# Kernel tuning notes

Hardware: AMD Instinct MI355X
Metric: run time of the kernel (lower is better)

## Reference

```python
import jax, jax.numpy as jnp
import numpy as np

NUM_HEADS = 16

def setup_inputs() -> dict:
    key = jax.random.key(0)
    ks = jax.random.split(key, 7)
    B, N, D = 2, 2048, 1024
    x = jax.random.normal(ks[0], (B, N, D), dtype=jnp.float32)
    gamma = jax.random.uniform(ks[1], (B, NUM_HEADS), dtype=jnp.float32)
    dist_matrix = jax.random.uniform(ks[2], (N, N), dtype=jnp.float32)
    W_qkv = jax.random.normal(ks[3], (D, 3 * D), dtype=jnp.float32) * (D ** -0.5)
    b_qkv = jnp.zeros((3 * D,), dtype=jnp.float32)
    W_proj = jax.random.normal(ks[4], (D, D), dtype=jnp.float32) * (D ** -0.5)
    b_proj = jnp.zeros((D,), dtype=jnp.float32)
    return {"x": x, "gamma": gamma, "dist_matrix": dist_matrix,
            "W_qkv": W_qkv, "b_qkv": b_qkv, "W_proj": W_proj, "b_proj": b_proj}

def reference(x, gamma, dist_matrix, W_qkv, b_qkv, W_proj, b_proj):
    B, N, D = x.shape
    H = NUM_HEADS
    hd = D // H
    scale = D ** -0.5  # standard_scale=False -> dim**-0.5
    # qkv projection: [B,N,3D] -> [3,B,H,N,hd]
    qkv = (x @ W_qkv + b_qkv).reshape(B, N, 3, H, hd).transpose(2, 0, 3, 1, 4)
    q, k, v = qkv[0], qkv[1], qkv[2]
    # scores with zoom bias: [B,H,N,N]
    scores = jnp.einsum('bhnd,bhmd->bhnm', q, k) * scale
    scores = scores - gamma[:, :, None, None] * dist_matrix[None, None, :, :]
    attn = jax.nn.softmax(scores, axis=-1)
    out = jnp.einsum('bhnm,bhmd->bhnd', attn, v)  # [B,H,N,hd]
    out = out.transpose(0, 2, 1, 3).reshape(B, N, D)
    return out @ W_proj + b_proj
```

## Files before the change

kernel.cpp:

```cpp
#include <hip/hip_runtime.h>
#include <cstdint>
#include <cstddef>

#define HD 64
#define NH 16
#define BATCH 2
#define SEQ 2048
#define DIM 1024
#define SCALE 0.03125f
#define LOG2E 1.4426950408889634f
#define QSCALE (SCALE * LOG2E)
#define NT (SEQ / 64)

typedef short bf16x8 __attribute__((ext_vector_type(8)));
typedef float f32x4 __attribute__((ext_vector_type(4)));
typedef unsigned u32x2 __attribute__((ext_vector_type(2)));
typedef unsigned u32x4 __attribute__((ext_vector_type(4)));

#define GL16(gp, lp) __builtin_amdgcn_global_load_lds( \
    (const __attribute__((address_space(1))) unsigned int*)(gp), \
    (__attribute__((address_space(3))) unsigned int*)(lp), 16, 0, 0)

static __device__ __forceinline__ unsigned short f2bf(float f) {
  union { float f; unsigned u; } a; a.f = f;
  unsigned r = a.u + 0x7fffu + ((a.u >> 16) & 1u);
  return (unsigned short)(r >> 16);
}

static __device__ __forceinline__ f32x4 zero4() {
  f32x4 z; z[0] = 0.f; z[1] = 0.f; z[2] = 0.f; z[3] = 0.f; return z;
}

__global__ void convert_x(const float* __restrict__ in, unsigned short* __restrict__ out, int n4) {
  int i = blockIdx.x * blockDim.x + threadIdx.x;
  if (i < n4) {
    float4 v = reinterpret_cast<const float4*>(in)[i];
    ushort4 o;
    o.x = f2bf(v.x); o.y = f2bf(v.y); o.z = f2bf(v.z); o.w = f2bf(v.w);
    reinterpret_cast<ushort4*>(out)[i] = o;
  }
}

__global__ void transpose_convert(const float* __restrict__ in, unsigned short* __restrict__ out,
                                  int R, int C) {
  __shared__ float tile[32][33];
  int bx = blockIdx.x * 32;
  int by = blockIdx.y * 32;
  int tx = threadIdx.x, ty = threadIdx.y;
  #pragma unroll
  for (int i = 0; i < 32; i += 8)
    tile[ty + i][tx] = in[(size_t)(by + ty + i) * C + bx + tx];
  __syncthreads();
  #pragma unroll
  for (int i = 0; i < 32; i += 8)
    out[(size_t)(bx + ty + i) * R + by + tx] = f2bf(tile[tx][ty + i]);
}

__global__ __launch_bounds__(256) void gemm128(
    const unsigned short* __restrict__ A, const unsigned short* __restrict__ Bt,
    const float* __restrict__ bias, int K, int mode,
    unsigned short* __restrict__ qo, unsigned short* __restrict__ ko,
    unsigned short* __restrict__ vo, float* __restrict__ outf) {
  __shared__ __attribute__((aligned(16))) unsigned short As[128 * 64];
  __shared__ __attribute__((aligned(16))) unsigned short Bs[128 * 64];
  const int tid = threadIdx.x;
  const int lane = tid & 63, w = tid >> 6;
  const int lo = lane & 15, hi = lane >> 4;
  const int wm = w >> 1, wn = w & 1;
  const int m0 = blockIdx.y * 128, n0 = blockIdx.x * 128;
  const int srow = tid >> 3, scol = (tid & 7) * 8;
  const unsigned short* abase = A + (size_t)(m0 + srow) * K + scol;
  const unsigned short* bbase = Bt + (size_t)(n0 + srow) * K + scol;

  f32x4 acc[4][4];
  #pragma unroll
  for (int mr = 0; mr < 4; ++mr)
    #pragma unroll
    for (int nr = 0; nr < 4; ++nr) acc[mr][nr] = zero4();

  const int nkt = K / 64;
  for (int kt = 0; kt < nkt; ++kt) {
    const unsigned short* ak = abase + kt * 64;
    const unsigned short* bk = bbase + kt * 64;
    #pragma unroll
    for (int i = 0; i < 4; ++i) {
      GL16(ak + (size_t)(32 * i) * K, &As[(w * 64 + 256 * i) * 8]);
      GL16(bk + (size_t)(32 * i) * K, &Bs[(w * 64 + 256 * i) * 8]);
    }
    __syncthreads();
    __builtin_amdgcn_s_setprio(1);
    #pragma unroll
    for (int kc = 0; kc < 2; ++kc) {
      bf16x8 af[4], bfr[4];
      #pragma unroll
      for (int mr = 0; mr < 4; ++mr)
        af[mr] = *reinterpret_cast<const bf16x8*>(
            &As[(wm * 64 + mr * 16 + lo) * 64 + kc * 32 + hi * 8]);
      #pragma unroll
      for (int nr = 0; nr < 4; ++nr)
        bfr[nr] = *reinterpret_cast<const bf16x8*>(
            &Bs[(wn * 64 + nr * 16 + lo) * 64 + kc * 32 + hi * 8]);
      #pragma unroll
      for (int mr = 0; mr < 4; ++mr)
        #pragma unroll
        for (int nr = 0; nr < 4; ++nr)
          acc[mr][nr] = __builtin_amdgcn_mfma_f32_16x16x32_bf16(af[mr], bfr[nr], acc[mr][nr], 0, 0, 0);
    }
    __builtin_amdgcn_s_setprio(0);
    __syncthreads();
  }

  #pragma unroll
  for (int nr = 0; nr < 4; ++nr) {
    const int gcol = n0 + wn * 64 + nr * 16 + lo;
    const float bv = bias[gcol];
    #pragma unroll
    for (int mr = 0; mr < 4; ++mr)
      #pragma unroll
      for (int j = 0; j < 4; ++j) {
        const int grow = m0 + wm * 64 + mr * 16 + hi * 4 + j;
        float val = acc[mr][nr][j] + bv;
        if (mode == 0) {
          int which = gcol >> 10;
          int hh = (gcol >> 6) & 15;
          int d = gcol & 63;
          int bb = grow >> 11;
          int n = grow & 2047;
          if (which == 0) {
            qo[((size_t)(bb * NH + hh) * SEQ + n) * HD + d] = f2bf(val * QSCALE);
          } else if (which == 1) {
            ko[((size_t)(bb * NH + hh) * SEQ + n) * HD + d] = f2bf(val);
          } else {
            vo[((size_t)(bb * NH + hh) * HD + d) * SEQ + n] = f2bf(val);
          }
        } else {
          outf[(size_t)grow * DIM + gcol] = val;
        }
      }
  }
}

__global__ __launch_bounds__(256, 4) void attn_kernel(
    const unsigned short* __restrict__ qb, const unsigned short* __restrict__ kb,
    const unsigned short* __restrict__ vtb, const float* __restrict__ gamma,
    const float* __restrict__ dist, unsigned short* __restrict__ ab) {
  __shared__ __attribute__((aligned(16))) unsigned short Ks[2][64 * 64];
  __shared__ __attribute__((aligned(16))) unsigned short Vt[2][64 * 64];
  __shared__ __attribute__((aligned(16))) unsigned short Ps[4 * 16 * 64];
  const int tid = threadIdx.x;
  const int lane = tid & 63;
  const int w = tid >> 6;
  const int lo = lane & 15;
  const int hi = lane >> 4;
  const int idx = blockIdx.x;
  const int bh = idx & 31;
  const int qt = idx >> 5;
  const int b = bh >> 4, h = bh & 15;
  const int qrow0 = qt * 64 + w * 16;
  const float g2 = gamma[bh] * LOG2E;

  const size_t base = (size_t)bh * SEQ * HD;
  const size_t vtbase = (size_t)bh * HD * SEQ;

  bf16x8 qf[2];
  #pragma unroll
  for (int kc = 0; kc < 2; ++kc)
    qf[kc] = *reinterpret_cast<const bf16x8*>(
        &qb[base + (size_t)(qrow0 + lo) * HD + kc * 32 + hi * 8]);

  const float* drow = dist + (size_t)(qrow0 + lo) * SEQ + hi * 4;

  f32x4 o[4];
  #pragma unroll
  for (int db = 0; db < 4; ++db) o[db] = zero4();
  float m_run = -INFINITY;
  float l_run = 0.f;

  const int srow = tid >> 3;
  const int schunk = (tid & 7) ^ (srow & 7);
  const unsigned short* ksrc0 = kb + base + (size_t)srow * HD + schunk * 8;
  const unsigned short* ksrc1 = ksrc0 + (size_t)32 * HD;
  const unsigned short* vsrc0 = vtb + vtbase + (size_t)srow * SEQ + schunk * 8;
  const unsigned short* vsrc1 = vsrc0 + (size_t)32 * SEQ;

  unsigned short* const psw = &Ps[w * 1024 + lo * 64];

  f32x4 dvA[4], dvB[4];

  GL16(ksrc0, &Ks[0][w * 512]);
  GL16(ksrc1, &Ks[0][2048 + w * 512]);
  GL16(vsrc0, &Vt[0][w * 512]);
  GL16(vsrc1, &Vt[0][2048 + w * 512]);
  #pragma unroll
  for (int nb = 0; nb < 4; ++nb)
    dvA[nb] = *reinterpret_cast<const f32x4*>(drow + nb * 16);
  __syncthreads();

#define TILE_BODY(CUR, NXT, MT, DVC, DVN)                                              \
  {                                                                                    \
    if ((MT) + 1 < NT) {                                                               \
      const int m1_ = ((MT) + 1) * 64;                                                 \
      GL16(ksrc0 + (size_t)m1_ * HD, &Ks[NXT][w * 512]);                               \
      GL16(ksrc1 + (size_t)m1_ * HD, &Ks[NXT][2048 + w * 512]);                        \
      GL16(vsrc0 + m1_, &Vt[NXT][w * 512]);                                            \
      GL16(vsrc1 + m1_, &Vt[NXT][2048 + w * 512]);                                     \
      _Pragma("unroll")                                                                \
      for (int nb = 0; nb < 4; ++nb)                                                   \
        DVN[nb] = *reinterpret_cast<const f32x4*>(drow + m1_ + nb * 16);               \
    }                                                                                  \
    f32x4 s[4];                                                                        \
    _Pragma("unroll")                                                                  \
    for (int nb = 0; nb < 4; ++nb) s[nb] = zero4();                                    \
    __builtin_amdgcn_s_setprio(1);                                                     \
    _Pragma("unroll")                                                                  \
    for (int nb = 0; nb < 4; ++nb)                                                     \
      _Pragma("unroll")                                                                \
      for (int kc = 0; kc < 2; ++kc) {                                                 \
        bf16x8 kf = *reinterpret_cast<const bf16x8*>(                                  \
            &Ks[CUR][(nb * 16 + lo) * 64 + ((kc * 4 + hi) ^ (lo & 7)) * 8]);           \
        s[nb] = __builtin_amdgcn_mfma_f32_16x16x32_bf16(kf, qf[kc], s[nb], 0, 0, 0);   \
      }                                                                                \
    __builtin_amdgcn_s_setprio(0);                                                     \
    float pm = -INFINITY;                                                              \
    _Pragma("unroll")                                                                  \
    for (int nb = 0; nb < 4; ++nb)                                                     \
      _Pragma("unroll")                                                                \
      for (int j = 0; j < 4; ++j) {                                                    \
        float v_ = __builtin_fmaf(-g2, DVC[nb][j], s[nb][j]);                          \
        s[nb][j] = v_;                                                                 \
        pm = fmaxf(pm, v_);                                                            \
      }                                                                                \
    pm = fmaxf(pm, __shfl_xor(pm, 16, 64));                                            \
    pm = fmaxf(pm, __shfl_xor(pm, 32, 64));                                            \
    if (!__all(pm <= m_run + 8.0f)) {                                                  \
      float mn_ = fmaxf(m_run, pm);                                                    \
      float corr_ = exp2f(m_run - mn_);                                                \
      m_run = mn_;                                                                     \
      l_run *= corr_;                                                                  \
      _Pragma("unroll")                                                                \
      for (int db = 0; db < 4; ++db) {                                                 \
        o[db][0] *= corr_; o[db][1] *= corr_;                                          \
        o[db][2] *= corr_; o[db][3] *= corr_;                                          \
      }                                                                                \
    }                                                                                  \
    float psum = 0.f;                                                                  \
    _Pragma("unroll")                                                                  \
    for (int nb = 0; nb < 4; ++nb) {                                                   \
      float p0 = exp2f(s[nb][0] - m_run);                                              \
      float p1 = exp2f(s[nb][1] - m_run);                                              \
      float p2 = exp2f(s[nb][2] - m_run);                                              \
      float p3 = exp2f(s[nb][3] - m_run);                                              \
      psum += (p0 + p1) + (p2 + p3);                                                   \
      unsigned pk0, pk1;                                                               \
      asm("v_cvt_pk_bf16_f32 %0, %1, %2" : "=v"(pk0) : "v"(p0), "v"(p1));              \
      asm("v_cvt_pk_bf16_f32 %0, %1, %2" : "=v"(pk1) : "v"(p2), "v"(p3));              \
      u32x2 pw_; pw_[0] = pk0; pw_[1] = pk1;                                           \
      *reinterpret_cast<u32x2*>(&psw[(((nb << 2) + hi) ^ lo) * 4]) = pw_;              \
    }                                                                                  \
    psum += __shfl_xor(psum, 16, 64);                                                  \
    psum += __shfl_xor(psum, 32, 64);                                                  \
    l_run += psum;                                                                     \
    __builtin_amdgcn_s_setprio(1);                                                     \
    _Pragma("unroll")                                                                  \
    for (int kc = 0; kc < 2; ++kc) {                                                   \
      u32x2 ra = *reinterpret_cast<const u32x2*>(&psw[(((kc << 3) + hi * 2) ^ lo) * 4]); \
      u32x2 rb = *reinterpret_cast<const u32x2*>(&psw[(((kc << 3) + hi * 2 + 1) ^ lo) * 4]); \
      u32x4 t_; t_[0] = ra[0]; t_[1] = ra[1]; t_[2] = rb[0]; t_[3] = rb[1];            \
      bf16x8 pf = __builtin_bit_cast(bf16x8, t_);                                      \
      _Pragma("unroll")                                                                \
      for (int db = 0; db < 4; ++db) {                                                 \
        bf16x8 vtf = *reinterpret_cast<const bf16x8*>(                                 \
            &Vt[CUR][(db * 16 + lo) * 64 + ((kc * 4 + hi) ^ (lo & 7)) * 8]);           \
        o[db] = __builtin_amdgcn_mfma_f32_16x16x32_bf16(vtf, pf, o[db], 0, 0, 0);      \
      }                                                                                \
    }                                                                                  \
    __builtin_amdgcn_s_setprio(0);                                                     \
    __syncthreads();                                                                   \
  }

  for (int mt = 0; mt < NT; mt += 2) {
    TILE_BODY(0, 1, mt, dvA, dvB)
    TILE_BODY(1, 0, mt + 1, dvB, dvA)
  }
#undef TILE_BODY

  {
    float rl = 1.0f / l_run;
    size_t row = (size_t)b * SEQ + qrow0 + lo;
    #pragma unroll
    for (int db = 0; db < 4; ++db) {
      ushort4 w4;
      w4.x = f2bf(o[db][0] * rl);
      w4.y = f2bf(o[db][1] * rl);
      w4.z = f2bf(o[db][2] * rl);
      w4.w = f2bf(o[db][3] * rl);
      *reinterpret_cast<ushort4*>(&ab[row * DIM + h * HD + db * 16 + hi * 4]) = w4;
    }
  }
}

extern "C" void kernel_launch(void* const* d_in, const int* in_sizes, int n_in,
                              void* d_out, int out_size, void* d_ws, size_t ws_size,
                              hipStream_t stream) {
  const float* x     = (const float*)d_in[0];
  const float* gamma = (const float*)d_in[1];
  const float* dist  = (const float*)d_in[2];
  const float* Wqkv  = (const float*)d_in[3];
  const float* bqkv  = (const float*)d_in[4];
  const float* Wproj = (const float*)d_in[5];
  const float* bproj = (const float*)d_in[6];
  float* out = (float*)d_out;

  char* ws = (char*)d_ws;
  unsigned short* xb     = (unsigned short*)(ws);
  unsigned short* wqkvt  = (unsigned short*)(ws + 8388608);
  unsigned short* wprojt = (unsigned short*)(ws + 14680064);
  unsigned short* qbuf   = (unsigned short*)(ws + 16777216);
  unsigned short* kbuf   = (unsigned short*)(ws + 25165824);
  unsigned short* vtbuf  = (unsigned short*)(ws + 33554432);
  unsigned short* abuf   = (unsigned short*)(ws + 41943040);

  convert_x<<<4096, 256, 0, stream>>>(x, xb, (BATCH * SEQ * DIM) / 4);
  transpose_convert<<<dim3(96, 32), dim3(32, 8), 0, stream>>>(Wqkv, wqkvt, DIM, 3 * DIM);
  transpose_convert<<<dim3(32, 32), dim3(32, 8), 0, stream>>>(Wproj, wprojt, DIM, DIM);
  gemm128<<<dim3(24, 32), 256, 0, stream>>>(xb, wqkvt, bqkv, DIM, 0, qbuf, kbuf, vtbuf, nullptr);
  attn_kernel<<<(SEQ / 64) * BATCH * NH, 256, 0, stream>>>(qbuf, kbuf, vtbuf, gamma, dist, abuf);
  gemm128<<<dim3(8, 32), 256, 0, stream>>>(abuf, wprojt, bproj, DIM, 1, nullptr, nullptr, nullptr, out);
}
```

Baseline: 172.4 us.

## Switch attention to 32x32x16 MFMA with register-resident P via permlane swap

```diff
diff --git a/kernel.cpp b/kernel.cpp
--- a/kernel.cpp
+++ b/kernel.cpp
@@ -14,7 +14,7 @@
 
 typedef short bf16x8 __attribute__((ext_vector_type(8)));
 typedef float f32x4 __attribute__((ext_vector_type(4)));
-typedef unsigned u32x2 __attribute__((ext_vector_type(2)));
+typedef float f32x16 __attribute__((ext_vector_type(16)));
 typedef unsigned u32x4 __attribute__((ext_vector_type(4)));
 
 #define GL16(gp, lp) __builtin_amdgcn_global_load_lds( \
@@ -140,39 +140,38 @@
   }
 }
 
-__global__ __launch_bounds__(256, 4) void attn_kernel(
+__global__ __launch_bounds__(256, 2) void attn_kernel(
     const unsigned short* __restrict__ qb, const unsigned short* __restrict__ kb,
     const unsigned short* __restrict__ vtb, const float* __restrict__ gamma,
     const float* __restrict__ dist, unsigned short* __restrict__ ab) {
   __shared__ __attribute__((aligned(16))) unsigned short Ks[2][64 * 64];
   __shared__ __attribute__((aligned(16))) unsigned short Vt[2][64 * 64];
-  __shared__ __attribute__((aligned(16))) unsigned short Ps[4 * 16 * 64];
   const int tid = threadIdx.x;
   const int lane = tid & 63;
   const int w = tid >> 6;
-  const int lo = lane & 15;
-  const int hi = lane >> 4;
+  const int q5 = lane & 31;
+  const int h5 = lane >> 5;
   const int idx = blockIdx.x;
   const int bh = idx & 31;
   const int qt = idx >> 5;
   const int b = bh >> 4, h = bh & 15;
-  const int qrow0 = qt * 64 + w * 16;
+  const int qrow0 = qt * 128 + w * 32;
   const float g2 = gamma[bh] * LOG2E;
 
   const size_t base = (size_t)bh * SEQ * HD;
   const size_t vtbase = (size_t)bh * HD * SEQ;
 
-  bf16x8 qf[2];
-  #pragma unroll
-  for (int kc = 0; kc < 2; ++kc)
-    qf[kc] = *reinterpret_cast<const bf16x8*>(
-        &qb[base + (size_t)(qrow0 + lo) * HD + kc * 32 + hi * 8]);
-
-  const float* drow = dist + (size_t)(qrow0 + lo) * SEQ + hi * 4;
-
-  f32x4 o[4];
-  #pragma unroll
-  for (int db = 0; db < 4; ++db) o[db] = zero4();
+  bf16x8 qf[4];
+  #pragma unroll
+  for (int ks = 0; ks < 4; ++ks)
+    qf[ks] = *reinterpret_cast<const bf16x8*>(
+        &qb[base + (size_t)(qrow0 + q5) * HD + ks * 16 + h5 * 8]);
+
+  const float* drow = dist + (size_t)(qrow0 + q5) * SEQ + 4 * h5;
+
+  f32x16 o[2];
+  #pragma unroll
+  for (int i = 0; i < 16; ++i) { o[0][i] = 0.f; o[1][i] = 0.f; }
   float m_run = -INFINITY;
   float l_run = 0.f;
 
@@ -183,119 +182,140 @@
   const unsigned short* vsrc0 = vtb + vtbase + (size_t)srow * SEQ + schunk * 8;
   const unsigned short* vsrc1 = vsrc0 + (size_t)32 * SEQ;
 
-  unsigned short* const psw = &Ps[w * 1024 + lo * 64];
-
-  f32x4 dvA[4], dvB[4];
+  f32x4 dv[2][4];
+  #pragma unroll
+  for (int blk = 0; blk < 2; ++blk)
+    #pragma unroll
+    for (int rp = 0; rp < 4; ++rp)
+      dv[blk][rp] = *reinterpret_cast<const f32x4*>(drow + 32 * blk + 8 * rp);
 
   GL16(ksrc0, &Ks[0][w * 512]);
   GL16(ksrc1, &Ks[0][2048 + w * 512]);
   GL16(vsrc0, &Vt[0][w * 512]);
   GL16(vsrc1, &Vt[0][2048 + w * 512]);
-  #pragma unroll
-  for (int nb = 0; nb < 4; ++nb)
-    dvA[nb] = *reinterpret_cast<const f32x4*>(drow + nb * 16);
   __syncthreads();
 
-#define TILE_BODY(CUR, NXT, MT, DVC, DVN)                                              \
-  {                                                                                    \
-    if ((MT) + 1 < NT) {                                                               \
-      const int m1_ = ((MT) + 1) * 64;                                                 \
-      GL16(ksrc0 + (size_t)m1_ * HD, &Ks[NXT][w * 512]);                               \
-      GL16(ksrc1 + (size_t)m1_ * HD, &Ks[NXT][2048 + w * 512]);                        \
-      GL16(vsrc0 + m1_, &Vt[NXT][w * 512]);                                            \
-      GL16(vsrc1 + m1_, &Vt[NXT][2048 + w * 512]);                                     \
-      _Pragma("unroll")                                                                \
-      for (int nb = 0; nb < 4; ++nb)                                                   \
-        DVN[nb] = *reinterpret_cast<const f32x4*>(drow + m1_ + nb * 16);               \
-    }                                                                                  \
-    f32x4 s[4];                                                                        \
-    _Pragma("unroll")                                                                  \
-    for (int nb = 0; nb < 4; ++nb) s[nb] = zero4();                                    \
-    __builtin_amdgcn_s_setprio(1);                                                     \
-    _Pragma("unroll")                                                                  \
-    for (int nb = 0; nb < 4; ++nb)                                                     \
-      _Pragma("unroll")                                                                \
-      for (int kc = 0; kc < 2; ++kc) {                                                 \
-        bf16x8 kf = *reinterpret_cast<const bf16x8*>(                                  \
-            &Ks[CUR][(nb * 16 + lo) * 64 + ((kc * 4 + hi) ^ (lo & 7)) * 8]);           \
-        s[nb] = __builtin_amdgcn_mfma_f32_16x16x32_bf16(kf, qf[kc], s[nb], 0, 0, 0);   \
-      }                                                                                \
-    __builtin_amdgcn_s_setprio(0);                                                     \
-    float pm = -INFINITY;                                                              \
-    _Pragma("unroll")                                                                  \
-    for (int nb = 0; nb < 4; ++nb)                                                     \
-      _Pragma("unroll")                                                                \
-      for (int j = 0; j < 4; ++j) {                                                    \
-        float v_ = __builtin_fmaf(-g2, DVC[nb][j], s[nb][j]);                          \
-        s[nb][j] = v_;                                                                 \
-        pm = fmaxf(pm, v_);                                                            \
-      }                                                                                \
-    pm = fmaxf(pm, __shfl_xor(pm, 16, 64));                                            \
-    pm = fmaxf(pm, __shfl_xor(pm, 32, 64));                                            \
-    if (!__all(pm <= m_run + 8.0f)) {                                                  \
-      float mn_ = fmaxf(m_run, pm);                                                    \
-      float corr_ = exp2f(m_run - mn_);                                                \
-      m_run = mn_;                                                                     \
-      l_run *= corr_;                                                                  \
-      _Pragma("unroll")                                                                \
-      for (int db = 0; db < 4; ++db) {                                                 \
-        o[db][0] *= corr_; o[db][1] *= corr_;                                          \
-        o[db][2] *= corr_; o[db][3] *= corr_;                                          \
-      }                                                                                \
-    }                                                                                  \
-    float psum = 0.f;                                                                  \
-    _Pragma("unroll")                                                                  \
-    for (int nb = 0; nb < 4; ++nb) {                                                   \
-      float p0 = exp2f(s[nb][0] - m_run);                                              \
-      float p1 = exp2f(s[nb][1] - m_run);                                              \
-      float p2 = exp2f(s[nb][2] - m_run);                                              \
-      float p3 = exp2f(s[nb][3] - m_run);                                              \
-      psum += (p0 + p1) + (p2 + p3);                                                   \
-      unsigned pk0, pk1;                                                               \
-      asm("v_cvt_pk_bf16_f32 %0, %1, %2" : "=v"(pk0) : "v"(p0), "v"(p1));              \
-      asm("v_cvt_pk_bf16_f32 %0, %1, %2" : "=v"(pk1) : "v"(p2), "v"(p3));              \
-      u32x2 pw_; pw_[0] = pk0; pw_[1] = pk1;                                           \
-      *reinterpret_cast<u32x2*>(&psw[(((nb << 2) + hi) ^ lo) * 4]) = pw_;              \
-    }                                                                                  \
-    psum += __shfl_xor(psum, 16, 64);                                                  \
-    psum += __shfl_xor(psum, 32, 64);                                                  \
-    l_run += psum;                                                                     \
-    __builtin_amdgcn_s_setprio(1);                                                     \
-    _Pragma("unroll")                                                                  \
-    for (int kc = 0; kc < 2; ++kc) {                                                   \
-      u32x2 ra = *reinterpret_cast<const u32x2*>(&psw[(((kc << 3) + hi * 2) ^ lo) * 4]); \
-      u32x2 rb = *reinterpret_cast<const u32x2*>(&psw[(((kc << 3) + hi * 2 + 1) ^ lo) * 4]); \
-      u32x4 t_; t_[0] = ra[0]; t_[1] = ra[1]; t_[2] = rb[0]; t_[3] = rb[1];            \
-      bf16x8 pf = __builtin_bit_cast(bf16x8, t_);                                      \
-      _Pragma("unroll")                                                                \
-      for (int db = 0; db < 4; ++db) {                                                 \
-        bf16x8 vtf = *reinterpret_cast<const bf16x8*>(                                 \
-            &Vt[CUR][(db * 16 + lo) * 64 + ((kc * 4 + hi) ^ (lo & 7)) * 8]);           \
-        o[db] = __builtin_amdgcn_mfma_f32_16x16x32_bf16(vtf, pf, o[db], 0, 0, 0);      \
-      }                                                                                \
-    }                                                                                  \
-    __builtin_amdgcn_s_setprio(0);                                                     \
-    __syncthreads();                                                                   \
-  }
-
-  for (int mt = 0; mt < NT; mt += 2) {
-    TILE_BODY(0, 1, mt, dvA, dvB)
-    TILE_BODY(1, 0, mt + 1, dvB, dvA)
-  }
-#undef TILE_BODY
+  for (int mt = 0; mt < NT; ++mt) {
+    const int cur = mt & 1;
+    if (mt + 1 < NT) {
+      const int m1 = (mt + 1) * 64;
+      GL16(ksrc0 + (size_t)m1 * HD, &Ks[cur ^ 1][w * 512]);
+      GL16(ksrc1 + (size_t)m1 * HD, &Ks[cur ^ 1][2048 + w * 512]);
+      GL16(vsrc0 + m1, &Vt[cur ^ 1][w * 512]);
+      GL16(vsrc1 + m1, &Vt[cur ^ 1][2048 + w * 512]);
+    }
+
+    f32x16 s[2];
+    #pragma unroll
+    for (int i = 0; i < 16; ++i) { s[0][i] = 0.f; s[1][i] = 0.f; }
+    __builtin_amdgcn_s_setprio(1);
+    #pragma unroll
+    for (int blk = 0; blk < 2; ++blk)
+      #pragma unroll
+      for (int ks = 0; ks < 4; ++ks) {
+        bf16x8 kf = *reinterpret_cast<const bf16x8*>(
+            &Ks[cur][(blk * 32 + q5) * 64 + ((ks * 2 + h5) ^ (q5 & 7)) * 8]);
+        s[blk] = __builtin_amdgcn_mfma_f32_32x32x16_bf16(kf, qf[ks], s[blk], 0, 0, 0);
+      }
+    __builtin_amdgcn_s_setprio(0);
+
+    float mx[8];
+    #pragma unroll
+    for (int blk = 0; blk < 2; ++blk)
+      #pragma unroll
+      for (int rp = 0; rp < 4; ++rp) {
+        float v0 = __builtin_fmaf(-g2, dv[blk][rp][0], s[blk][rp * 4 + 0]);
+        float v1 = __builtin_fmaf(-g2, dv[blk][rp][1], s[blk][rp * 4 + 1]);
+        float v2 = __builtin_fmaf(-g2, dv[blk][rp][2], s[blk][rp * 4 + 2]);
+        float v3 = __builtin_fmaf(-g2, dv[blk][rp][3], s[blk][rp * 4 + 3]);
+        s[blk][rp * 4 + 0] = v0; s[blk][rp * 4 + 1] = v1;
+        s[blk][rp * 4 + 2] = v2; s[blk][rp * 4 + 3] = v3;
+        mx[blk * 4 + rp] = fmaxf(fmaxf(v0, v1), fmaxf(v2, v3));
+      }
+    float pm = fmaxf(fmaxf(fmaxf(mx[0], mx[1]), fmaxf(mx[2], mx[3])),
+                     fmaxf(fmaxf(mx[4], mx[5]), fmaxf(mx[6], mx[7])));
+    pm = fmaxf(pm, __shfl_xor(pm, 32, 64));
+
+    if (mt + 1 < NT) {
+      const float* dn = drow + (mt + 1) * 64;
+      #pragma unroll
+      for (int blk = 0; blk < 2; ++blk)
+        #pragma unroll
+        for (int rp = 0; rp < 4; ++rp)
+          dv[blk][rp] = *reinterpret_cast<const f32x4*>(dn + 32 * blk + 8 * rp);
+    }
+
+    if (!__all(pm <= m_run + 8.0f)) {
+      float mn = fmaxf(m_run, pm);
+      float corr = exp2f(m_run - mn);
+      m_run = mn;
+      l_run *= corr;
+      #pragma unroll
+      for (int i = 0; i < 16; ++i) { o[0][i] *= corr; o[1][i] *= corr; }
+    }
+
+    float psum = 0.f;
+    unsigned u[2][4][2];
+    #pragma unroll
+    for (int blk = 0; blk < 2; ++blk)
+      #pragma unroll
+      for (int rp = 0; rp < 4; ++rp) {
+        float p0 = exp2f(s[blk][rp * 4 + 0] - m_run);
+        float p1 = exp2f(s[blk][rp * 4 + 1] - m_run);
+        float p2 = exp2f(s[blk][rp * 4 + 2] - m_run);
+        float p3 = exp2f(s[blk][rp * 4 + 3] - m_run);
+        psum += (p0 + p1) + (p2 + p3);
+        asm("v_cvt_pk_bf16_f32 %0, %1, %2" : "=v"(u[blk][rp][0]) : "v"(p0), "v"(p1));
+        asm("v_cvt_pk_bf16_f32 %0, %1, %2" : "=v"(u[blk][rp][1]) : "v"(p2), "v"(p3));
+      }
+    psum += __shfl_xor(psum, 32, 64);
+    l_run += psum;
+
+    unsigned pu[4][4];
+    #pragma unroll
+    for (int blk = 0; blk < 2; ++blk)
+      #pragma unroll
+      for (int jp = 0; jp < 2; ++jp) {
+        unsigned a0 = u[blk][0][jp], b0 = u[blk][1][jp];
+        asm("v_permlane32_swap_b32 %0, %1" : "+v"(a0), "+v"(b0));
+        pu[2 * blk][jp] = a0; pu[2 * blk][2 + jp] = b0;
+        unsigned a1 = u[blk][2][jp], b1 = u[blk][3][jp];
+        asm("v_permlane32_swap_b32 %0, %1" : "+v"(a1), "+v"(b1));
+        pu[2 * blk + 1][jp] = a1; pu[2 * blk + 1][2 + jp] = b1;
+      }
+
+    __builtin_amdgcn_s_setprio(1);
+    #pragma unroll
+    for (int ks = 0; ks < 4; ++ks) {
+      u32x4 t; t[0] = pu[ks][0]; t[1] = pu[ks][1]; t[2] = pu[ks][2]; t[3] = pu[ks][3];
+      bf16x8 pf = __builtin_bit_cast(bf16x8, t);
+      #pragma unroll
+      for (int db = 0; db < 2; ++db) {
+        bf16x8 vtf = *reinterpret_cast<const bf16x8*>(
+            &Vt[cur][(db * 32 + q5) * 64 + ((ks * 2 + h5) ^ (q5 & 7)) * 8]);
+        o[db] = __builtin_amdgcn_mfma_f32_32x32x16_bf16(vtf, pf, o[db], 0, 0, 0);
+      }
+    }
+    __builtin_amdgcn_s_setprio(0);
+
+    __syncthreads();
+  }
 
   {
     float rl = 1.0f / l_run;
-    size_t row = (size_t)b * SEQ + qrow0 + lo;
-    #pragma unroll
-    for (int db = 0; db < 4; ++db) {
-      ushort4 w4;
-      w4.x = f2bf(o[db][0] * rl);
-      w4.y = f2bf(o[db][1] * rl);
-      w4.z = f2bf(o[db][2] * rl);
-      w4.w = f2bf(o[db][3] * rl);
-      *reinterpret_cast<ushort4*>(&ab[row * DIM + h * HD + db * 16 + hi * 4]) = w4;
-    }
+    size_t row = (size_t)b * SEQ + qrow0 + q5;
+    unsigned short* obase = ab + row * DIM + h * HD + 4 * h5;
+    #pragma unroll
+    for (int db = 0; db < 2; ++db)
+      #pragma unroll
+      for (int rp = 0; rp < 4; ++rp) {
+        ushort4 w4;
+        w4.x = f2bf(o[db][rp * 4 + 0] * rl);
+        w4.y = f2bf(o[db][rp * 4 + 1] * rl);
+        w4.z = f2bf(o[db][rp * 4 + 2] * rl);
+        w4.w = f2bf(o[db][rp * 4 + 3] * rl);
+        *reinterpret_cast<ushort4*>(&obase[db * 32 + 8 * rp]) = w4;
+      }
   }
 }
 
@@ -324,6 +344,6 @@
   transpose_convert<<<dim3(96, 32), dim3(32, 8), 0, stream>>>(Wqkv, wqkvt, DIM, 3 * DIM);
   transpose_convert<<<dim3(32, 32), dim3(32, 8), 0, stream>>>(Wproj, wprojt, DIM, DIM);
   gemm128<<<dim3(24, 32), 256, 0, stream>>>(xb, wqkvt, bqkv, DIM, 0, qbuf, kbuf, vtbuf, nullptr);
-  attn_kernel<<<(SEQ / 64) * BATCH * NH, 256, 0, stream>>>(qbuf, kbuf, vtbuf, gamma, dist, abuf);
+  attn_kernel<<<(SEQ / 128) * BATCH * NH, 256, 0, stream>>>(qbuf, kbuf, vtbuf, gamma, dist, abuf);
   gemm128<<<dim3(8, 32), 256, 0, stream>>>(abuf, wprojt, bproj, DIM, 1, nullptr, nullptr, nullptr, out);
 }
```

Measured after the change: 173.8 us. No clear change (+0.8%).

## Rework attention around 32x32 MFMA with register P and software-pipelined QK

Applied to the files above, without the earlier changes.

```diff
diff --git a/kernel.cpp b/kernel.cpp
--- a/kernel.cpp
+++ b/kernel.cpp
@@ -14,7 +14,7 @@
 
 typedef short bf16x8 __attribute__((ext_vector_type(8)));
 typedef float f32x4 __attribute__((ext_vector_type(4)));
-typedef unsigned u32x2 __attribute__((ext_vector_type(2)));
+typedef float f32x16 __attribute__((ext_vector_type(16)));
 typedef unsigned u32x4 __attribute__((ext_vector_type(4)));
 
 #define GL16(gp, lp) __builtin_amdgcn_global_load_lds( \
@@ -67,7 +67,11 @@
   const int lane = tid & 63, w = tid >> 6;
   const int lo = lane & 15, hi = lane >> 4;
   const int wm = w >> 1, wn = w & 1;
-  const int m0 = blockIdx.y * 128, n0 = blockIdx.x * 128;
+  const int gx = gridDim.x;
+  const int nwg = gx * gridDim.y;
+  const int flat = blockIdx.y * gx + blockIdx.x;
+  const int swz = (flat & 7) * (nwg >> 3) + (flat >> 3);
+  const int m0 = (swz / gx) * 128, n0 = (swz % gx) * 128;
   const int srow = tid >> 3, scol = (tid & 7) * 8;
   const unsigned short* abase = A + (size_t)(m0 + srow) * K + scol;
   const unsigned short* bbase = Bt + (size_t)(n0 + srow) * K + scol;
@@ -140,39 +144,38 @@
   }
 }
 
-__global__ __launch_bounds__(256, 4) void attn_kernel(
+__global__ __launch_bounds__(256, 2) void attn_kernel(
     const unsigned short* __restrict__ qb, const unsigned short* __restrict__ kb,
     const unsigned short* __restrict__ vtb, const float* __restrict__ gamma,
     const float* __restrict__ dist, unsigned short* __restrict__ ab) {
   __shared__ __attribute__((aligned(16))) unsigned short Ks[2][64 * 64];
   __shared__ __attribute__((aligned(16))) unsigned short Vt[2][64 * 64];
-  __shared__ __attribute__((aligned(16))) unsigned short Ps[4 * 16 * 64];
   const int tid = threadIdx.x;
   const int lane = tid & 63;
   const int w = tid >> 6;
-  const int lo = lane & 15;
-  const int hi = lane >> 4;
+  const int q5 = lane & 31;
+  const int h5 = lane >> 5;
   const int idx = blockIdx.x;
   const int bh = idx & 31;
   const int qt = idx >> 5;
   const int b = bh >> 4, h = bh & 15;
-  const int qrow0 = qt * 64 + w * 16;
+  const int qrow0 = qt * 128 + w * 32;
   const float g2 = gamma[bh] * LOG2E;
 
   const size_t base = (size_t)bh * SEQ * HD;
   const size_t vtbase = (size_t)bh * HD * SEQ;
 
-  bf16x8 qf[2];
-  #pragma unroll
-  for (int kc = 0; kc < 2; ++kc)
-    qf[kc] = *reinterpret_cast<const bf16x8*>(
-        &qb[base + (size_t)(qrow0 + lo) * HD + kc * 32 + hi * 8]);
-
-  const float* drow = dist + (size_t)(qrow0 + lo) * SEQ + hi * 4;
-
-  f32x4 o[4];
-  #pragma unroll
-  for (int db = 0; db < 4; ++db) o[db] = zero4();
+  bf16x8 qf[4];
+  #pragma unroll
+  for (int ks = 0; ks < 4; ++ks)
+    qf[ks] = *reinterpret_cast<const bf16x8*>(
+        &qb[base + (size_t)(qrow0 + q5) * HD + ks * 16 + h5 * 8]);
+
+  const float* drow = dist + (size_t)(qrow0 + q5) * SEQ + 4 * h5;
+
+  f32x16 o[2];
+  #pragma unroll
+  for (int i = 0; i < 16; ++i) { o[0][i] = 0.f; o[1][i] = 0.f; }
   float m_run = -INFINITY;
   float l_run = 0.f;
 
@@ -183,95 +186,131 @@
   const unsigned short* vsrc0 = vtb + vtbase + (size_t)srow * SEQ + schunk * 8;
   const unsigned short* vsrc1 = vsrc0 + (size_t)32 * SEQ;
 
-  unsigned short* const psw = &Ps[w * 1024 + lo * 64];
-
-  f32x4 dvA[4], dvB[4];
-
   GL16(ksrc0, &Ks[0][w * 512]);
   GL16(ksrc1, &Ks[0][2048 + w * 512]);
   GL16(vsrc0, &Vt[0][w * 512]);
   GL16(vsrc1, &Vt[0][2048 + w * 512]);
-  #pragma unroll
-  for (int nb = 0; nb < 4; ++nb)
-    dvA[nb] = *reinterpret_cast<const f32x4*>(drow + nb * 16);
+  GL16(ksrc0 + (size_t)64 * HD, &Ks[1][w * 512]);
+  GL16(ksrc1 + (size_t)64 * HD, &Ks[1][2048 + w * 512]);
   __syncthreads();
 
-#define TILE_BODY(CUR, NXT, MT, DVC, DVN)                                              \
+  f32x16 sA[2], sB[2];
+
+  #pragma unroll
+  for (int i = 0; i < 16; ++i) { sA[0][i] = 0.f; sA[1][i] = 0.f; }
+  __builtin_amdgcn_s_setprio(1);
+  #pragma unroll
+  for (int blk = 0; blk < 2; ++blk)
+    #pragma unroll
+    for (int ks = 0; ks < 4; ++ks) {
+      bf16x8 kf = *reinterpret_cast<const bf16x8*>(
+          &Ks[0][(blk * 32 + q5) * 64 + ((ks * 2 + h5) ^ (q5 & 7)) * 8]);
+      sA[blk] = __builtin_amdgcn_mfma_f32_32x32x16_bf16(kf, qf[ks], sA[blk], 0, 0, 0);
+    }
+  __builtin_amdgcn_s_setprio(0);
+  __syncthreads();
+
+#define ITER(T, CUR, SCUR, SNXT)                                                       \
   {                                                                                    \
-    if ((MT) + 1 < NT) {                                                               \
-      const int m1_ = ((MT) + 1) * 64;                                                 \
-      GL16(ksrc0 + (size_t)m1_ * HD, &Ks[NXT][w * 512]);                               \
-      GL16(ksrc1 + (size_t)m1_ * HD, &Ks[NXT][2048 + w * 512]);                        \
-      GL16(vsrc0 + m1_, &Vt[NXT][w * 512]);                                            \
-      GL16(vsrc1 + m1_, &Vt[NXT][2048 + w * 512]);                                     \
-      _Pragma("unroll")                                                                \
-      for (int nb = 0; nb < 4; ++nb)                                                   \
-        DVN[nb] = *reinterpret_cast<const f32x4*>(drow + m1_ + nb * 16);               \
-    }                                                                                  \
-    f32x4 s[4];                                                                        \
+                         \
+    f32x4 dv[2][4];                                                                    \
+    { const float* dp = drow + (T) * 64;                                               \
+      _Pragma("unroll")                                                                \
+      for (int blk = 0; blk < 2; ++blk)                                                \
+        _Pragma("unroll")                                                              \
+        for (int rp = 0; rp < 4; ++rp)                                                 \
+          dv[blk][rp] = *reinterpret_cast<const f32x4*>(dp + 32 * blk + 8 * rp);       \
+    }                                                                                  \
+         \
+    if ((T) + 1 < NT) {                                                                \
+      _Pragma("unroll")                                                                \
+      for (int i = 0; i < 16; ++i) { SNXT[0][i] = 0.f; SNXT[1][i] = 0.f; }             \
+      __builtin_amdgcn_s_setprio(1);                                                   \
+      _Pragma("unroll")                                                                \
+      for (int blk = 0; blk < 2; ++blk)                                                \
+        _Pragma("unroll")                                                              \
+        for (int ks = 0; ks < 4; ++ks) {                                               \
+          bf16x8 kf = *reinterpret_cast<const bf16x8*>(                                \
+              &Ks[(CUR) ^ 1][(blk * 32 + q5) * 64 + ((ks * 2 + h5) ^ (q5 & 7)) * 8]);  \
+          SNXT[blk] = __builtin_amdgcn_mfma_f32_32x32x16_bf16(kf, qf[ks], SNXT[blk], 0, 0, 0); \
+        }                                                                              \
+      __builtin_amdgcn_s_setprio(0);                                                   \
+    }                                                                                  \
+           \
+    if ((T) + 2 < NT) {                                                                \
+      const size_t m2 = (size_t)((T) + 2) * 64;                                        \
+      GL16(ksrc0 + m2 * HD, &Ks[CUR][w * 512]);                                        \
+      GL16(ksrc1 + m2 * HD, &Ks[CUR][2048 + w * 512]);                                 \
+    }                                                                                  \
+    if ((T) + 1 < NT) {                                                                \
+      const int m1 = ((T) + 1) * 64;                                                   \
+      GL16(vsrc0 + m1, &Vt[(CUR) ^ 1][w * 512]);                                       \
+      GL16(vsrc1 + m1, &Vt[(CUR) ^ 1][2048 + w * 512]);                                \
+    }                                                                                  \
+                           \
+    float mx[8];                                                                       \
     _Pragma("unroll")                                                                  \
-    for (int nb = 0; nb < 4; ++nb) s[nb] = zero4();                                    \
+    for (int blk = 0; blk < 2; ++blk)                                                  \
+      _Pragma("unroll")                                                                \
+      for (int rp = 0; rp < 4; ++rp) {                                                 \
+        float v0 = __builtin_fmaf(-g2, dv[blk][rp][0], SCUR[blk][rp * 4 + 0]);         \
+        float v1 = __builtin_fmaf(-g2, dv[blk][rp][1], SCUR[blk][rp * 4 + 1]);         \
+        float v2 = __builtin_fmaf(-g2, dv[blk][rp][2], SCUR[blk][rp * 4 + 2]);         \
+        float v3 = __builtin_fmaf(-g2, dv[blk][rp][3], SCUR[blk][rp * 4 + 3]);         \
+        SCUR[blk][rp * 4 + 0] = v0; SCUR[blk][rp * 4 + 1] = v1;                        \
+        SCUR[blk][rp * 4 + 2] = v2; SCUR[blk][rp * 4 + 3] = v3;                        \
+        mx[blk * 4 + rp] = fmaxf(fmaxf(v0, v1), fmaxf(v2, v3));                        \
+      }                                                                                \
+    float pm = fmaxf(fmaxf(fmaxf(mx[0], mx[1]), fmaxf(mx[2], mx[3])),                  \
+                     fmaxf(fmaxf(mx[4], mx[5]), fmaxf(mx[6], mx[7])));                 \
+    pm = fmaxf(pm, __shfl_xor(pm, 32, 64));                                            \
+    if (!__all(pm <= m_run + 8.0f)) {                                                  \
+      float mn = fmaxf(m_run, pm);                                                     \
+      float corr = exp2f(m_run - mn);                                                  \
+      m_run = mn;                                                                      \
+      l_run *= corr;                                                                   \
+      _Pragma("unroll")                                                                \
+      for (int i = 0; i < 16; ++i) { o[0][i] *= corr; o[1][i] *= corr; }               \
+    }                                                                                  \
+    float psum = 0.f;                                                                  \
+    unsigned u[2][4][2];                                                               \
+    _Pragma("unroll")                                                                  \
+    for (int blk = 0; blk < 2; ++blk)                                                  \
+      _Pragma("unroll")                                                                \
+      for (int rp = 0; rp < 4; ++rp) {                                                 \
+        float p0 = exp2f(SCUR[blk][rp * 4 + 0] - m_run);                               \
+        float p1 = exp2f(SCUR[blk][rp * 4 + 1] - m_run);                               \
+        float p2 = exp2f(SCUR[blk][rp * 4 + 2] - m_run);                               \
+        float p3 = exp2f(SCUR[blk][rp * 4 + 3] - m_run);                               \
+        psum += (p0 + p1) + (p2 + p3);                                                 \
+        asm("v_cvt_pk_bf16_f32 %0, %1, %2" : "=v"(u[blk][rp][0]) : "v"(p0), "v"(p1));  \
+        asm("v_cvt_pk_bf16_f32 %0, %1, %2" : "=v"(u[blk][rp][1]) : "v"(p2), "v"(p3));  \
+      }                                                                                \
+    psum += __shfl_xor(psum, 32, 64);                                                  \
+    l_run += psum;                                                                     \
+    unsigned pu[4][4];                                                                 \
+    _Pragma("unroll")                                                                  \
+    for (int blk = 0; blk < 2; ++blk)                                                  \
+      _Pragma("unroll")                                                                \
+      for (int jp = 0; jp < 2; ++jp) {                                                 \
+        unsigned a0 = u[blk][0][jp], b0 = u[blk][1][jp];                               \
+        asm("v_permlane32_swap_b32 %0, %1" : "+v"(a0), "+v"(b0));                      \
+        pu[2 * blk][jp] = a0; pu[2 * blk][2 + jp] = b0;                                \
+        unsigned a1 = u[blk][2][jp], b1 = u[blk][3][jp];                               \
+        asm("v_permlane32_swap_b32 %0, %1" : "+v"(a1), "+v"(b1));                      \
+        pu[2 * blk + 1][jp] = a1; pu[2 * blk + 1][2 + jp] = b1;                        \
+      }                                                                                \
+                                                               \
     __builtin_amdgcn_s_setprio(1);                                                     \
     _Pragma("unroll")                                                                  \
-    for (int nb = 0; nb < 4; ++nb)                                                     \
-      _Pragma("unroll")                                                                \
-      for (int kc = 0; kc < 2; ++kc) {                                                 \
-        bf16x8 kf = *reinterpret_cast<const bf16x8*>(                                  \
-            &Ks[CUR][(nb * 16 + lo) * 64 + ((kc * 4 + hi) ^ (lo & 7)) * 8]);           \
-        s[nb] = __builtin_amdgcn_mfma_f32_16x16x32_bf16(kf, qf[kc], s[nb], 0, 0, 0);   \
-      }                                                                                \
-    __builtin_amdgcn_s_setprio(0);                                                     \
-    float pm = -INFINITY;                                                              \
-    _Pragma("unroll")                                                                  \
-    for (int nb = 0; nb < 4; ++nb)                                                     \
-      _Pragma("unroll")                                                                \
-      for (int j = 0; j < 4; ++j) {                                                    \
-        float v_ = __builtin_fmaf(-g2, DVC[nb][j], s[nb][j]);                          \
-        s[nb][j] = v_;                                                                 \
-        pm = fmaxf(pm, v_);                                                            \
-      }                                                                                \
-    pm = fmaxf(pm, __shfl_xor(pm, 16, 64));                                            \
-    pm = fmaxf(pm, __shfl_xor(pm, 32, 64));                                            \
-    if (!__all(pm <= m_run + 8.0f)) {                                                  \
-      float mn_ = fmaxf(m_run, pm);                                                    \
-      float corr_ = exp2f(m_run - mn_);                                                \
-      m_run = mn_;                                                                     \
-      l_run *= corr_;                                                                  \
-      _Pragma("unroll")                                                                \
-      for (int db = 0; db < 4; ++db) {                                                 \
-        o[db][0] *= corr_; o[db][1] *= corr_;                                          \
-        o[db][2] *= corr_; o[db][3] *= corr_;                                          \
-      }                                                                                \
-    }                                                                                  \
-    float psum = 0.f;                                                                  \
-    _Pragma("unroll")                                                                  \
-    for (int nb = 0; nb < 4; ++nb) {                                                   \
-      float p0 = exp2f(s[nb][0] - m_run);                                              \
-      float p1 = exp2f(s[nb][1] - m_run);                                              \
-      float p2 = exp2f(s[nb][2] - m_run);                                              \
-      float p3 = exp2f(s[nb][3] - m_run);                                              \
-      psum += (p0 + p1) + (p2 + p3);                                                   \
-      unsigned pk0, pk1;                                                               \
-      asm("v_cvt_pk_bf16_f32 %0, %1, %2" : "=v"(pk0) : "v"(p0), "v"(p1));              \
-      asm("v_cvt_pk_bf16_f32 %0, %1, %2" : "=v"(pk1) : "v"(p2), "v"(p3));              \
-      u32x2 pw_; pw_[0] = pk0; pw_[1] = pk1;                                           \
-      *reinterpret_cast<u32x2*>(&psw[(((nb << 2) + hi) ^ lo) * 4]) = pw_;              \
-    }                                                                                  \
-    psum += __shfl_xor(psum, 16, 64);                                                  \
-    psum += __shfl_xor(psum, 32, 64);                                                  \
-    l_run += psum;                                                                     \
-    __builtin_amdgcn_s_setprio(1);                                                     \
-    _Pragma("unroll")                                                                  \
-    for (int kc = 0; kc < 2; ++kc) {                                                   \
-      u32x2 ra = *reinterpret_cast<const u32x2*>(&psw[(((kc << 3) + hi * 2) ^ lo) * 4]); \
-      u32x2 rb = *reinterpret_cast<const u32x2*>(&psw[(((kc << 3) + hi * 2 + 1) ^ lo) * 4]); \
-      u32x4 t_; t_[0] = ra[0]; t_[1] = ra[1]; t_[2] = rb[0]; t_[3] = rb[1];            \
+    for (int ks = 0; ks < 4; ++ks) {                                                   \
+      u32x4 t_; t_[0] = pu[ks][0]; t_[1] = pu[ks][1]; t_[2] = pu[ks][2]; t_[3] = pu[ks][3]; \
       bf16x8 pf = __builtin_bit_cast(bf16x8, t_);                                      \
       _Pragma("unroll")                                                                \
-      for (int db = 0; db < 4; ++db) {                                                 \
+      for (int db = 0; db < 2; ++db) {                                                 \
         bf16x8 vtf = *reinterpret_cast<const bf16x8*>(                                 \
-            &Vt[CUR][(db * 16 + lo) * 64 + ((kc * 4 + hi) ^ (lo & 7)) * 8]);           \
-        o[db] = __builtin_amdgcn_mfma_f32_16x16x32_bf16(vtf, pf, o[db], 0, 0, 0);      \
+            &Vt[CUR][(db * 32 + q5) * 64 + ((ks * 2 + h5) ^ (q5 & 7)) * 8]);           \
+        o[db] = __builtin_amdgcn_mfma_f32_32x32x16_bf16(vtf, pf, o[db], 0, 0, 0);      \
       }                                                                                \
     }                                                                                  \
     __builtin_amdgcn_s_setprio(0);                                                     \
@@ -279,23 +318,26 @@
   }
 
   for (int mt = 0; mt < NT; mt += 2) {
-    TILE_BODY(0, 1, mt, dvA, dvB)
-    TILE_BODY(1, 0, mt + 1, dvB, dvA)
-  }
-#undef TILE_BODY
+    ITER(mt, 0, sA, sB)
+    ITER(mt + 1, 1, sB, sA)
+  }
+#undef ITER
 
   {
     float rl = 1.0f / l_run;
-    size_t row = (size_t)b * SEQ + qrow0 + lo;
-    #pragma unroll
-    for (int db = 0; db < 4; ++db) {
-      ushort4 w4;
-      w4.x = f2bf(o[db][0] * rl);
-      w4.y = f2bf(o[db][1] * rl);
-      w4.z = f2bf(o[db][2] * rl);
-      w4.w = f2bf(o[db][3] * rl);
-      *reinterpret_cast<ushort4*>(&ab[row * DIM + h * HD + db * 16 + hi * 4]) = w4;
-    }
+    size_t row = (size_t)b * SEQ + qrow0 + q5;
+    unsigned short* obase = ab + row * DIM + h * HD + 4 * h5;
+    #pragma unroll
+    for (int db = 0; db < 2; ++db)
+      #pragma unroll
+      for (int rp = 0; rp < 4; ++rp) {
+        ushort4 w4;
+        w4.x = f2bf(o[db][rp * 4 + 0] * rl);
+        w4.y = f2bf(o[db][rp * 4 + 1] * rl);
+        w4.z = f2bf(o[db][rp * 4 + 2] * rl);
+        w4.w = f2bf(o[db][rp * 4 + 3] * rl);
+        *reinterpret_cast<ushort4*>(&obase[db * 32 + 8 * rp]) = w4;
+      }
   }
 }
 
@@ -324,6 +366,6 @@
   transpose_convert<<<dim3(96, 32), dim3(32, 8), 0, stream>>>(Wqkv, wqkvt, DIM, 3 * DIM);
   transpose_convert<<<dim3(32, 32), dim3(32, 8), 0, stream>>>(Wproj, wprojt, DIM, DIM);
   gemm128<<<dim3(24, 32), 256, 0, stream>>>(xb, wqkvt, bqkv, DIM, 0, qbuf, kbuf, vtbuf, nullptr);
-  attn_kernel<<<(SEQ / 64) * BATCH * NH, 256, 0, stream>>>(qbuf, kbuf, vtbuf, gamma, dist, abuf);
+  attn_kernel<<<(SEQ / 128) * BATCH * NH, 256, 0, stream>>>(qbuf, kbuf, vtbuf, gamma, dist, abuf);
   gemm128<<<dim3(8, 32), 256, 0, stream>>>(abuf, wprojt, bproj, DIM, 1, nullptr, nullptr, nullptr, out);
 }
```

After: 175.2 us. About the same (+1.6%).
